# Performance work log

Hardware: AMD Instinct MI355X
Metric: run time of the kernel (lower is better)

## Reference

```python
import jax, jax.numpy as jnp
import numpy as np
from jax import lax

X_SIZE, Z_SIZE, H, GC, PD = 256, 64, 64, 16, 2
B, K, T = 256, 16, 50
LOG_SIG_MIN, LOG_SIG_MAX, LOG_P_MAX = -10.0, 10.0, 50.0
ZX = X_SIZE + Z_SIZE
LSTM_IN = ZX + PD


def setup_inputs() -> dict:
    key = jax.random.key(0)
    ks = jax.random.split(key, 24)
    s = lambda fan_in: 1.0 / np.sqrt(fan_in)
    u = lambda k, shape, sc: jax.random.uniform(k, shape, jnp.float32, -sc, sc)
    inp = {
        'x': jax.random.normal(ks[0], (B, X_SIZE), jnp.float32),
        'z_stacked': jax.random.normal(ks[1], (K, B, Z_SIZE), jnp.float32),
        'input_seqs': jax.random.normal(ks[2], (B, 8, 2, 2, 6), jnp.float32),
        'pred_seqs': jax.random.normal(ks[3], (B, T, 2, 2, 6), jnp.float32),
        # initial_h / initial_c linears: ZX -> H
        'Wh0': u(ks[4], (H, ZX), s(ZX)), 'bh0': u(ks[5], (H,), s(ZX)),
        'Wc0': u(ks[6], (H, ZX), s(ZX)), 'bc0': u(ks[7], (H,), s(ZX)),
        # LSTMCell: gates order i,f,g,o
        'Wih': u(ks[8], (4 * H, LSTM_IN), s(H)), 'Whh': u(ks[9], (4 * H, H), s(H)),
        'bih': u(ks[10], (4 * H,), s(H)), 'bhh': u(ks[11], (4 * H,), s(H)),
        # GMM parameter heads: H -> GC / GC*PD
        'Wpi': u(ks[12], (GC, H), s(H)), 'bpi': u(ks[13], (GC,), s(H)),
        'Wmu': u(ks[14], (GC * PD, H), s(H)), 'bmu': u(ks[15], (GC * PD,), s(H)),
        'Wls': u(ks[16], (GC * PD, H), s(H)), 'bls': u(ks[17], (GC * PD,), s(H)),
        'Wcorr': u(ks[18], (GC, H), s(H)), 'bcorr': u(ks[19], (GC,), s(H)),
        'n_z_samples': K,
    }
    return inp


def _gmm2d_log_prob(log_pis, mus, log_sigmas, corrs, value):
    # log_pis/corrs: [K,B,T,GC]; mus/log_sigmas: [K,B,T,GC*PD]; value: [B,T,PD]
    ls = jnp.clip(log_sigmas, LOG_SIG_MIN, LOG_SIG_MAX).reshape(K, B, T, GC, PD)
    mu = mus.reshape(K, B, T, GC, PD)
    dx = value[None, :, :, None, :] - mu                      # [K,B,T,GC,PD]
    zscore = dx * jnp.exp(-ls)                                # dx / sigma
    one_m_rho2 = 1.0 - corrs ** 2
    quad = (zscore[..., 0] ** 2 + zscore[..., 1] ** 2
            - 2.0 * corrs * zscore[..., 0] * zscore[..., 1])
    comp = (-jnp.log(2.0 * jnp.pi) - ls.sum(-1)
            - 0.5 * jnp.log(one_m_rho2) - 0.5 * quad / one_m_rho2)
    log_pi_n = jax.nn.log_softmax(log_pis, axis=-1)
    log_p_t = jax.nn.logsumexp(log_pi_n + comp, axis=-1)      # [K,B,T]
    return jnp.minimum(log_p_t, LOG_P_MAX)


def reference(x, z_stacked, input_seqs, pred_seqs,
              Wh0, bh0, Wc0, bc0, Wih, Whh, bih, bhh,
              Wpi, bpi, Wmu, bmu, Wls, bls, Wcorr, bcorr, n_z_samples):
    tgt_future = pred_seqs[:, :, 1, 1, 2:4]                   # [B,T,2]
    tgt_present = input_seqs[:, -1, 1, 1, 2:4]                # [B,2]
    z = z_stacked.reshape(-1, z_stacked.shape[-1])            # [K*B, z]
    zx = jnp.concatenate([z, jnp.tile(x, (n_z_samples, 1))], axis=1)  # [N, ZX]
    N = zx.shape[0]
    h0 = zx @ Wh0.T + bh0
    c0 = zx @ Wc0.T + bc0
    decode_inputs = jnp.concatenate([tgt_present[:, None, :], tgt_future[:, :T - 1, :]], axis=1)  # [B,T,2]
    inputs = jnp.concatenate([
        jnp.broadcast_to(zx[:, None, :], (N, T, ZX)),
        jnp.tile(decode_inputs, (n_z_samples, 1, 1))], axis=2)  # [N,T,ZX+2]

    def step(carry, xt):
        h, c = carry
        gates = xt @ Wih.T + bih + h @ Whh.T + bhh
        i, f, g, o = jnp.split(gates, 4, axis=-1)
        c = jax.nn.sigmoid(f) * c + jax.nn.sigmoid(i) * jnp.tanh(g)
        h = jax.nn.sigmoid(o) * jnp.tanh(c)
        return (h, c), h

    _, hs = lax.scan(step, (h0, c0), jnp.swapaxes(inputs, 0, 1))  # [T,N,H]
    hs = jnp.swapaxes(hs, 0, 1)                                   # [N,T,H]

    log_pis = (hs @ Wpi.T + bpi).reshape(K, B, T, GC)
    mus = (hs @ Wmu.T + bmu).reshape(K, B, T, GC * PD)
    log_sigmas = (hs @ Wls.T + bls).reshape(K, B, T, GC * PD)
    corrs = jnp.tanh(hs @ Wcorr.T + bcorr).reshape(K, B, T, GC)

    log_p_yt_xz = _gmm2d_log_prob(log_pis, mus, log_sigmas, corrs, tgt_future)
    return log_p_yt_xz.sum(axis=2)                                # [K,B]
```

## Files before the change

### kernel.cpp

```cpp
#include <hip/hip_runtime.h>


#define T_ 50

typedef __attribute__((ext_vector_type(8))) short short8;
typedef __attribute__((ext_vector_type(4))) float f32x4;

#define MFMA(a, b, c) __builtin_amdgcn_mfma_f32_16x16x32_bf16(a, b, c, 0, 0, 0)

#define HBYTES 26214400
#define WIH_B 0
#define WH0_B 20480
#define WC0_B 25600
#define WHH_B 30720
#define PRJ_B 34816

__device__ __forceinline__ float sigf(float x)  { return 1.0f / (1.0f + __expf(-x)); }
__device__ __forceinline__ float tanh_(float x) { return 1.0f - 2.0f / (__expf(2.0f * x) + 1.0f); }

__device__ __forceinline__ void splitf(float f, unsigned short& hi, unsigned short& lo) {
    unsigned b = __float_as_uint(f);
    hi = (unsigned short)(b >> 16);
    float fh = __uint_as_float(b & 0xffff0000u);
    lo = (unsigned short)(__float_as_uint(f - fh) >> 16);
}

__device__ __forceinline__ void pack8(const float* p, short8& hi, short8& lo) {
    #pragma unroll
    for (int e = 0; e < 8; ++e) {
        unsigned short h, l;
        splitf(p[e], h, l);
        hi[e] = (short)h; lo[e] = (short)l;
    }
}

__global__ void pack_kernel(const float* __restrict__ Wih, const float* __restrict__ Whh,
                            const float* __restrict__ Wh0, const float* __restrict__ Wc0,
                            const float* __restrict__ Wpi, const float* __restrict__ Wmu,
                            const float* __restrict__ Wls, const float* __restrict__ Wcorr,
                            short8* __restrict__ WF)
{
    int id = blockIdx.x * 256 + threadIdx.x;
    if (id >= 18176) return;
    const float* src;
    int dst0, dst1;
    if (id < 10240) {
        int ks = id >> 10, rem = id & 1023;
        int q = rem >> 8, rem2 = rem & 255;
        int w = rem2 >> 6, l = rem2 & 63;
        int g = l >> 4, c = l & 15;
        src = Wih + (q*64 + w*16 + c)*322 + ks*32 + g*8;
        dst0 = WIH_B + (((ks*4 + q)*2 + 0)*4 + w)*64 + l;
        dst1 = WIH_B + (((ks*4 + q)*2 + 1)*4 + w)*64 + l;
    } else if (id < 12800) {
        int t2 = id - 10240;
        int ks = t2 >> 8, rem = t2 & 255;
        int w = rem >> 6, l = rem & 63;
        int g = l >> 4, c = l & 15;
        src = Wh0 + (w*16 + c)*320 + ks*32 + g*8;
        dst0 = WH0_B + ((ks*2 + 0)*4 + w)*64 + l;
        dst1 = WH0_B + ((ks*2 + 1)*4 + w)*64 + l;
    } else if (id < 15360) {
        int t2 = id - 12800;
        int ks = t2 >> 8, rem = t2 & 255;
        int w = rem >> 6, l = rem & 63;
        int g = l >> 4, c = l & 15;
        src = Wc0 + (w*16 + c)*320 + ks*32 + g*8;
        dst0 = WC0_B + ((ks*2 + 0)*4 + w)*64 + l;
        dst1 = WC0_B + ((ks*2 + 1)*4 + w)*64 + l;
    } else if (id < 17408) {
        int t3 = id - 15360;
        int q = t3 >> 9, rem = t3 & 511;
        int ks = rem >> 8, rem2 = rem & 255;
        int w = rem2 >> 6, l = rem2 & 63;
        int g = l >> 4, c = l & 15;
        src = Whh + (q*64 + w*16 + c)*64 + ks*32 + g*8;
        dst0 = WHH_B + (((q*2 + ks)*2 + 0)*4 + w)*64 + l;
        dst1 = WHH_B + (((q*2 + ks)*2 + 1)*4 + w)*64 + l;
    } else {
        int t4 = id - 17408;
        int pt = t4 >> 7, rem = t4 & 127;
        int ks = rem >> 6, l = rem & 63;
        int g = l >> 4, c = l & 15;
        int r3 = pt*16 + c;
        const float* p;
        if      (r3 < 16) p = Wpi   + r3*64;
        else if (r3 < 48) p = Wmu   + (r3-16)*64;
        else if (r3 < 80) p = Wls   + (r3-48)*64;
        else              p = Wcorr + (r3-80)*64;
        src = p + ks*32 + g*8;
        dst0 = PRJ_B + ((pt*2 + ks)*2 + 0)*64 + l;
        dst1 = PRJ_B + ((pt*2 + ks)*2 + 1)*64 + l;
    }
    short8 hi, lo;
    pack8(src, hi, lo);
    WF[dst0] = hi;
    WF[dst1] = lo;
}

__launch_bounds__(256, 2)
__global__ void lstm_kernel(
    const float* __restrict__ x,        const float* __restrict__ z,
    const float* __restrict__ inp_seqs, const float* __restrict__ pred_seqs,
    const float* __restrict__ Wih,      const float* __restrict__ bh0,
    const float* __restrict__ bc0,      const float* __restrict__ bih,
    const float* __restrict__ bhh,
    unsigned short* __restrict__ Hout,  const short8* __restrict__ WF)
{
    __shared__ __align__(16) float smem[4560];
    float* ZXL = smem;
    unsigned short* HB = (unsigned short*)(smem + 2592);
    unsigned short* H0h = HB;
    unsigned short* H0l = HB + 576;
    unsigned short* H1h = HB + 1152;
    unsigned short* H1l = HB + 1728;
    float* FUT = smem + 3744;
    float* PRS = smem + 4544;

    const int j = threadIdx.x;
    const int w = j >> 6;
    const int l = j & 63;
    const int g = l >> 4;
    const int c = l & 15;
    const int U = w*16 + c;
    const int blk = blockIdx.x;

    for (int e = j; e < 8*320; e += 256) {
        int s = e / 320, k = e - s*320;
        int n = blk*8 + s, kk = n >> 8, b = n & 255;
        ZXL[s*324 + k] = (k < 64) ? z[(kk*256 + b)*64 + k] : x[b*256 + (k - 64)];
    }
    for (int e = j; e < T_*16; e += 256) {
        int t = e >> 4, s = (e >> 1) & 7;
        int b = (blk*8 + s) & 255;
        FUT[e] = pred_seqs[b*1200 + t*24 + 20 + (e & 1)];
    }
    if (j < 16) {
        int b = (blk*8 + (j >> 1)) & 255;
        PRS[j] = inp_seqs[b*192 + 188 + (j & 1)];
    }
    __syncthreads();

    const int R0 = U, R1 = 64+U, R2 = 128+U, R3 = 192+U;
    f32x4 gc[4], h0a, c0a;
    {
        float b0 = bih[R0]+bhh[R0], b1 = bih[R1]+bhh[R1];
        float b2 = bih[R2]+bhh[R2], b3 = bih[R3]+bhh[R3];
        gc[0] = (f32x4){b0,b0,b0,b0}; gc[1] = (f32x4){b1,b1,b1,b1};
        gc[2] = (f32x4){b2,b2,b2,b2}; gc[3] = (f32x4){b3,b3,b3,b3};
        float bh_ = bh0[U], bc_ = bc0[U];
        h0a = (f32x4){bh_,bh_,bh_,bh_};
        c0a = (f32x4){bc_,bc_,bc_,bc_};
    }
    for (int ks = 0; ks < 10; ++ks) {
        short8 ahi, alo;
        pack8(&ZXL[(c & 7)*324 + ks*32 + g*8], ahi, alo);
        #pragma unroll
        for (int q = 0; q < 4; ++q) {
            short8 Bh = WF[WIH_B + (((ks*4 + q)*2 + 0)*4 + w)*64 + l];
            short8 Bl = WF[WIH_B + (((ks*4 + q)*2 + 1)*4 + w)*64 + l];
            gc[q] = MFMA(ahi, Bh, gc[q]);
            gc[q] = MFMA(ahi, Bl, gc[q]);
            gc[q] = MFMA(alo, Bh, gc[q]);
        }
        {
            short8 Bh = WF[WH0_B + ((ks*2 + 0)*4 + w)*64 + l];
            short8 Bl = WF[WH0_B + ((ks*2 + 1)*4 + w)*64 + l];
            h0a = MFMA(ahi, Bh, h0a); h0a = MFMA(ahi, Bl, h0a); h0a = MFMA(alo, Bh, h0a);
        }
        {
            short8 Bh = WF[WC0_B + ((ks*2 + 0)*4 + w)*64 + l];
            short8 Bl = WF[WC0_B + ((ks*2 + 1)*4 + w)*64 + l];
            c0a = MFMA(ahi, Bh, c0a); c0a = MFMA(ahi, Bl, c0a); c0a = MFMA(alo, Bh, c0a);
        }
    }

    const bool lowg = (g < 2);
    const int s0 = 4*(g & 1) + (lowg ? 0 : 2);
    float cst0 = lowg ? c0a[0] : c0a[2];
    float cst1 = lowg ? c0a[1] : c0a[3];
    {
        float hv0 = lowg ? h0a[0] : h0a[2];
        float hv1 = lowg ? h0a[1] : h0a[3];
        unsigned short hh, ll;
        splitf(hv0, hh, ll); H0h[s0*72 + U] = hh; H0l[s0*72 + U] = ll;
        splitf(hv1, hh, ll); H0h[(s0+1)*72 + U] = hh; H0l[(s0+1)*72 + U] = ll;
    }

    float wd0[4], wd1[4];
    wd0[0] = Wih[R0*322+320]; wd1[0] = Wih[R0*322+321];
    wd0[1] = Wih[R1*322+320]; wd1[1] = Wih[R1*322+321];
    wd0[2] = Wih[R2*322+320]; wd1[2] = Wih[R2*322+321];
    wd0[3] = Wih[R3*322+320]; wd1[3] = Wih[R3*322+321];
    short8 WB[4][2][2];
    #pragma unroll
    for (int q = 0; q < 4; ++q)
        #pragma unroll
        for (int ks = 0; ks < 2; ++ks)
            #pragma unroll
            for (int p = 0; p < 2; ++p)
                WB[q][ks][p] = WF[WHH_B + (((q*2 + ks)*2 + p)*4 + w)*64 + l];

    __syncthreads();

    const int nbase = blk*8;
    for (int t = 0; t < T_; ++t) {
        const unsigned short* Hh = (t & 1) ? H1h : H0h;
        const unsigned short* Hl = (t & 1) ? H1l : H0l;
        unsigned short* Nh = (t & 1) ? H0h : H1h;
        unsigned short* Nl = (t & 1) ? H0l : H1l;

        short8 ah0 = *reinterpret_cast<const short8*>(Hh + (c & 7)*72 + g*8);
        short8 al0 = *reinterpret_cast<const short8*>(Hl + (c & 7)*72 + g*8);
        short8 ah1 = *reinterpret_cast<const short8*>(Hh + (c & 7)*72 + 32 + g*8);
        short8 al1 = *reinterpret_cast<const short8*>(Hl + (c & 7)*72 + 32 + g*8);

        const float* dptr = (t == 0) ? PRS : (FUT + (t-1)*16);
        float2 dvr[4];
        #pragma unroll
        for (int r = 0; r < 4; ++r)
            dvr[r] = *reinterpret_cast<const float2*>(dptr + ((4*g + r) & 7)*2);

        f32x4 aq[4];
        #pragma unroll
        for (int q = 0; q < 4; ++q) {
            #pragma unroll
            for (int r = 0; r < 4; ++r)
                aq[q][r] = gc[q][r] + dvr[r].x*wd0[q] + dvr[r].y*wd1[q];
            aq[q] = MFMA(ah0, WB[q][0][0], aq[q]);
            aq[q] = MFMA(ah0, WB[q][0][1], aq[q]);
            aq[q] = MFMA(al0, WB[q][0][0], aq[q]);
            aq[q] = MFMA(ah1, WB[q][1][0], aq[q]);
            aq[q] = MFMA(ah1, WB[q][1][1], aq[q]);
            aq[q] = MFMA(al1, WB[q][1][0], aq[q]);
        }

        float i0 = lowg ? aq[0][0] : aq[0][2], i1 = lowg ? aq[0][1] : aq[0][3];
        float f0 = lowg ? aq[1][0] : aq[1][2], f1 = lowg ? aq[1][1] : aq[1][3];
        float g0 = lowg ? aq[2][0] : aq[2][2], g1 = lowg ? aq[2][1] : aq[2][3];
        float o0 = lowg ? aq[3][0] : aq[3][2], o1 = lowg ? aq[3][1] : aq[3][3];
        float cc0 = sigf(f0)*cst0 + sigf(i0)*tanh_(g0); cst0 = cc0;
        float cc1 = sigf(f1)*cst1 + sigf(i1)*tanh_(g1); cst1 = cc1;
        float hv0 = sigf(o0)*tanh_(cc0);
        float hv1 = sigf(o1)*tanh_(cc1);

        unsigned short hh0, ll0, hh1, ll1;
        splitf(hv0, hh0, ll0);
        splitf(hv1, hh1, ll1);
        Hout[(size_t)(t*4096 + nbase + s0)*64 + U]     = hh0;
        Hout[(size_t)(t*4096 + nbase + s0 + 1)*64 + U] = hh1;
        Nh[s0*72 + U] = hh0;  Nl[s0*72 + U] = ll0;
        Nh[(s0+1)*72 + U] = hh1;  Nl[(s0+1)*72 + U] = ll1;
        __syncthreads();
    }
}

__launch_bounds__(256, 3)
__global__ void head_kernel(const float* __restrict__ pred_seqs,
                            const float* __restrict__ bpi, const float* __restrict__ bmu,
                            const float* __restrict__ bls, const float* __restrict__ bcorr,
                            const unsigned short* __restrict__ Hin,
                            const short8* __restrict__ WF,
                            float* __restrict__ out)
{
    __shared__ __align__(16) float PL[4][1600];
    const int j = threadIdx.x;
    const int w = j >> 6;
    const int l = j & 63;
    const int g = l >> 4;
    const int c = l & 15;
    const int blk = blockIdx.x;
    const int set = blk >> 2, chunk = blk & 3;
    const int t0 = (chunk*25) >> 1, t1 = ((chunk+1)*25) >> 1;

    float bias[6];
    #pragma unroll
    for (int pt = 0; pt < 6; ++pt) {
        int r3 = pt*16 + c;
        bias[pt] = (r3 < 16) ? bpi[r3] : (r3 < 48) ? bmu[r3-16]
                 : (r3 < 80) ? bls[r3-48] : bcorr[r3-80];
    }

    const int s = l >> 2, q4 = l & 3;
    const int n_s = set*16 + s, b_s = n_s & 255;
    float* PLw = &PL[w][0];
    float sum_local = 0.0f;

    for (int t = t0 + w; t < t1; t += 4) {
        const unsigned short* hp = Hin + (size_t)(t*4096 + set*16 + c)*64;
        short8 ah0 = *reinterpret_cast<const short8*>(hp + g*8);
        short8 ah1 = *reinterpret_cast<const short8*>(hp + 32 + g*8);
        #pragma unroll
        for (int pt = 0; pt < 6; ++pt) {
            short8 B00 = WF[PRJ_B + ((pt*2 + 0)*2 + 0)*64 + l];
            short8 B01 = WF[PRJ_B + ((pt*2 + 0)*2 + 1)*64 + l];
            short8 B10 = WF[PRJ_B + ((pt*2 + 1)*2 + 0)*64 + l];
            short8 B11 = WF[PRJ_B + ((pt*2 + 1)*2 + 1)*64 + l];
            f32x4 p = (f32x4){bias[pt], bias[pt], bias[pt], bias[pt]};
            p = MFMA(ah0, B00, p);
            p = MFMA(ah0, B01, p);
            p = MFMA(ah1, B10, p);
            p = MFMA(ah1, B11, p);
            #pragma unroll
            for (int r = 0; r < 4; ++r) PLw[(4*g + r)*100 + pt*16 + c] = p[r];
        }
        asm volatile("s_waitcnt lgkmcnt(0)" ::: "memory");
        __builtin_amdgcn_sched_barrier(0);

        float2 tv = *reinterpret_cast<const float2*>(pred_seqs + b_s*1200 + t*24 + 20);
        float a[4], m = -1e30f, Ppi = 0.0f;
        #pragma unroll
        for (int i = 0; i < 4; ++i) {
            int cq = q4*4 + i;
            float pi = PLw[s*100 + cq];
            float2 mu = *reinterpret_cast<const float2*>(PLw + s*100 + 16 + 2*cq);
            float2 ls = *reinterpret_cast<const float2*>(PLw + s*100 + 48 + 2*cq);
            float co = PLw[s*100 + 80 + cq];
            float l0 = fminf(fmaxf(ls.x, -10.0f), 10.0f);
            float l1 = fminf(fmaxf(ls.y, -10.0f), 10.0f);
            float z0 = (tv.x - mu.x) * __expf(-l0);
            float z1 = (tv.y - mu.y) * __expf(-l1);
            float ct = tanh_(co);
            float omr = 1.0f - ct*ct;
            float quad = z0*z0 + z1*z1 - 2.0f*ct*z0*z1;
            float comp = -1.8378770664093453f - (l0 + l1) - 0.5f*__logf(omr) - 0.5f*quad/omr;
            a[i] = pi + comp;
            m = fmaxf(m, a[i]);
            Ppi += __expf(pi);
        }
        m = fmaxf(m, __shfl_xor(m, 1));
        m = fmaxf(m, __shfl_xor(m, 2));
        float E = __expf(a[0]-m) + __expf(a[1]-m) + __expf(a[2]-m) + __expf(a[3]-m);
        E   += __shfl_xor(E, 1);   E   += __shfl_xor(E, 2);
        Ppi += __shfl_xor(Ppi, 1); Ppi += __shfl_xor(Ppi, 2);
        float logp = m + __logf(E) - __logf(Ppi);
        sum_local += fminf(logp, 50.0f);
    }
    if (q4 == 0) atomicAdd(out + n_s, sum_local);
}

extern "C" void kernel_launch(void* const* d_in, const int* in_sizes, int n_in,
                              void* d_out, int out_size, void* d_ws, size_t ws_size,
                              hipStream_t stream) {
    const float* x     = (const float*)d_in[0];
    const float* z     = (const float*)d_in[1];
    const float* iseq  = (const float*)d_in[2];
    const float* pseq  = (const float*)d_in[3];
    const float* Wh0   = (const float*)d_in[4];
    const float* bh0   = (const float*)d_in[5];
    const float* Wc0   = (const float*)d_in[6];
    const float* bc0   = (const float*)d_in[7];
    const float* Wih   = (const float*)d_in[8];
    const float* Whh   = (const float*)d_in[9];
    const float* bih   = (const float*)d_in[10];
    const float* bhh   = (const float*)d_in[11];
    const float* Wpi   = (const float*)d_in[12];
    const float* bpi   = (const float*)d_in[13];
    const float* Wmu   = (const float*)d_in[14];
    const float* bmu   = (const float*)d_in[15];
    const float* Wls   = (const float*)d_in[16];
    const float* bls   = (const float*)d_in[17];
    const float* Wcorr = (const float*)d_in[18];
    const float* bcorr = (const float*)d_in[19];
    float* out = (float*)d_out;

    unsigned short* Hbuf = (unsigned short*)d_ws;
    short8* WF = (short8*)((char*)d_ws + HBYTES);

    pack_kernel<<<71, 256, 0, stream>>>(Wih, Whh, Wh0, Wc0, Wpi, Wmu, Wls, Wcorr, WF);
    lstm_kernel<<<512, 256, 0, stream>>>(x, z, iseq, pseq, Wih, bh0, bc0, bih, bhh,
                                         Hbuf, (const short8*)WF);
    hipMemsetAsync(d_out, 0, 4096 * sizeof(float), stream);
    head_kernel<<<1024, 256, 0, stream>>>(pseq, bpi, bmu, bls, bcorr,
                                          (const unsigned short*)Hbuf,
                                          (const short8*)WF, out);
}
```

Measured before the change: 114.6 us.

## Split LSTM into prep GEMM kernel and per-wave recurrence without block barriers

Moves the input-projection and initial h/c GEMMs into a separate prep kernel that writes the gate constants, h0 and c0 to workspace, and packs only Whh and the head weights. The recurrence now gives each wave its own 4 sequences with all of Whh kept in registers, so the per-step __syncthreads is gone and only wave-local LDS sync remains. Each wave does 16 tiles of 6 MFMAs per step but uses only one row of each result, trading wasted MFMA work and heavy register pressure for no cross-wave synchronization. The recurrent grid halves to 256 blocks.

```diff
diff --git a/kernel.cpp b/kernel.cpp
--- a/kernel.cpp
+++ b/kernel.cpp
@@ -2,18 +2,16 @@
 
 
 #define T_ 50
-
 typedef __attribute__((ext_vector_type(8))) short short8;
 typedef __attribute__((ext_vector_type(4))) float f32x4;
-
-#define MFMA(a, b, c) __builtin_amdgcn_mfma_f32_16x16x32_bf16(a, b, c, 0, 0, 0)
-
-#define HBYTES 26214400
-#define WIH_B 0
-#define WH0_B 20480
-#define WC0_B 25600
-#define WHH_B 30720
-#define PRJ_B 34816
+#define MFMA(a,b,c) __builtin_amdgcn_mfma_f32_16x16x32_bf16(a,b,c,0,0,0)
+
+#define HOUT_B 0u
+#define GCT_B  26214400u
+#define H0_B   30408704u
+#define C0_B   31457280u
+#define WF_B   32505856u
+#define PRJ_SLOT 4096
 
 __device__ __forceinline__ float sigf(float x)  { return 1.0f / (1.0f + __expf(-x)); }
 __device__ __forceinline__ float tanh_(float x) { return 1.0f - 2.0f / (__expf(2.0f * x) + 1.0f); }
@@ -34,224 +32,209 @@
     }
 }
 
-__global__ void pack_kernel(const float* __restrict__ Wih, const float* __restrict__ Whh,
-                            const float* __restrict__ Wh0, const float* __restrict__ Wc0,
-                            const float* __restrict__ Wpi, const float* __restrict__ Wmu,
-                            const float* __restrict__ Wls, const float* __restrict__ Wcorr,
-                            short8* __restrict__ WF)
+union U8 { short8 s; unsigned u[4]; };
+
+__launch_bounds__(256, 1)
+__global__ void prep_kernel(
+    const float* __restrict__ x,   const float* __restrict__ z,
+    const float* __restrict__ Wh0, const float* __restrict__ bh0,
+    const float* __restrict__ Wc0, const float* __restrict__ bc0,
+    const float* __restrict__ Wih, const float* __restrict__ Whh,
+    const float* __restrict__ bih, const float* __restrict__ bhh,
+    const float* __restrict__ Wpi, const float* __restrict__ Wmu,
+    const float* __restrict__ Wls, const float* __restrict__ Wcorr,
+    float* __restrict__ gcT, unsigned* __restrict__ h0u32,
+    float* __restrict__ c0f, short8* __restrict__ WF)
 {
-    int id = blockIdx.x * 256 + threadIdx.x;
-    if (id >= 18176) return;
-    const float* src;
-    int dst0, dst1;
-    if (id < 10240) {
-        int ks = id >> 10, rem = id & 1023;
-        int q = rem >> 8, rem2 = rem & 255;
-        int w = rem2 >> 6, l = rem2 & 63;
-        int g = l >> 4, c = l & 15;
-        src = Wih + (q*64 + w*16 + c)*322 + ks*32 + g*8;
-        dst0 = WIH_B + (((ks*4 + q)*2 + 0)*4 + w)*64 + l;
-        dst1 = WIH_B + (((ks*4 + q)*2 + 1)*4 + w)*64 + l;
-    } else if (id < 12800) {
-        int t2 = id - 10240;
-        int ks = t2 >> 8, rem = t2 & 255;
-        int w = rem >> 6, l = rem & 63;
-        int g = l >> 4, c = l & 15;
-        src = Wh0 + (w*16 + c)*320 + ks*32 + g*8;
-        dst0 = WH0_B + ((ks*2 + 0)*4 + w)*64 + l;
-        dst1 = WH0_B + ((ks*2 + 1)*4 + w)*64 + l;
-    } else if (id < 15360) {
-        int t2 = id - 12800;
-        int ks = t2 >> 8, rem = t2 & 255;
-        int w = rem >> 6, l = rem & 63;
-        int g = l >> 4, c = l & 15;
-        src = Wc0 + (w*16 + c)*320 + ks*32 + g*8;
-        dst0 = WC0_B + ((ks*2 + 0)*4 + w)*64 + l;
-        dst1 = WC0_B + ((ks*2 + 1)*4 + w)*64 + l;
-    } else if (id < 17408) {
-        int t3 = id - 15360;
-        int q = t3 >> 9, rem = t3 & 511;
-        int ks = rem >> 8, rem2 = rem & 255;
-        int w = rem2 >> 6, l = rem2 & 63;
-        int g = l >> 4, c = l & 15;
-        src = Whh + (q*64 + w*16 + c)*64 + ks*32 + g*8;
-        dst0 = WHH_B + (((q*2 + ks)*2 + 0)*4 + w)*64 + l;
-        dst1 = WHH_B + (((q*2 + ks)*2 + 1)*4 + w)*64 + l;
-    } else {
-        int t4 = id - 17408;
-        int pt = t4 >> 7, rem = t4 & 127;
-        int ks = rem >> 6, l = rem & 63;
-        int g = l >> 4, c = l & 15;
-        int r3 = pt*16 + c;
-        const float* p;
-        if      (r3 < 16) p = Wpi   + r3*64;
-        else if (r3 < 48) p = Wmu   + (r3-16)*64;
-        else if (r3 < 80) p = Wls   + (r3-48)*64;
-        else              p = Wcorr + (r3-80)*64;
-        src = p + ks*32 + g*8;
-        dst0 = PRJ_B + ((pt*2 + ks)*2 + 0)*64 + l;
-        dst1 = PRJ_B + ((pt*2 + ks)*2 + 1)*64 + l;
-    }
-    short8 hi, lo;
-    pack8(src, hi, lo);
-    WF[dst0] = hi;
-    WF[dst1] = lo;
-}
-
-__launch_bounds__(256, 2)
+    const int j = threadIdx.x;
+    if (blockIdx.x >= 256) {
+        int tid = (blockIdx.x - 256)*256 + j;
+        if (tid < 2048) {
+            int lane = tid & 63, r = tid >> 6;
+            int ks = r & 1, tile = r >> 1;
+            int tau = tile >> 2, ublk = tile & 3;
+            int g = lane >> 4, c = lane & 15;
+            const float* src = Whh + (tau*64 + 16*ublk + c)*64 + ks*32 + g*8;
+            short8 hi, lo; pack8(src, hi, lo);
+            WF[(r*2 + 0)*64 + lane] = hi;
+            WF[(r*2 + 1)*64 + lane] = lo;
+        } else if (tid < 2816) {
+            int t2 = tid - 2048;
+            int lane = t2 & 63, r = t2 >> 6;
+            int ks = r & 1, pt = r >> 1;
+            int g = lane >> 4, c = lane & 15;
+            int r3 = pt*16 + c;
+            const float* p;
+            if      (r3 < 16) p = Wpi   + r3*64;
+            else if (r3 < 48) p = Wmu   + (r3-16)*64;
+            else if (r3 < 80) p = Wls   + (r3-48)*64;
+            else              p = Wcorr + (r3-80)*64;
+            short8 hi, lo; pack8(p + ks*32 + g*8, hi, lo);
+            WF[PRJ_SLOT + (r*2 + 0)*64 + lane] = hi;
+            WF[PRJ_SLOT + (r*2 + 1)*64 + lane] = lo;
+        }
+        return;
+    }
+
+    __shared__ __align__(16) float ZXL[16*324];
+    const int blk = blockIdx.x;
+    for (int e = j; e < 16*320; e += 256) {
+        int s = e / 320, k = e - s*320;
+        int n = blk*16 + s, b = n & 255;
+        ZXL[s*324 + k] = (k < 64) ? z[n*64 + k] : x[b*256 + (k - 64)];
+    }
+    __syncthreads();
+
+    const int w = j >> 6, l = j & 63, g = l >> 4, c = l & 15;
+    f32x4 acc[6];
+    const float* src[6];
+    #pragma unroll
+    for (int i = 0; i < 6; ++i) {
+        int T = w*6 + i;
+        float bias;
+        if (T < 16)      { int ga = T*16 + c;      bias = bih[ga] + bhh[ga]; src[i] = Wih + ga*322; }
+        else if (T < 20) { int u  = (T-16)*16 + c; bias = bh0[u];            src[i] = Wh0 + u*320; }
+        else             { int u  = (T-20)*16 + c; bias = bc0[u];            src[i] = Wc0 + u*320; }
+        acc[i] = (f32x4){bias, bias, bias, bias};
+    }
+    for (int ks = 0; ks < 10; ++ks) {
+        short8 ah, al;
+        pack8(&ZXL[c*324 + ks*32 + g*8], ah, al);
+        #pragma unroll
+        for (int i = 0; i < 6; ++i) {
+            short8 bh, bl;
+            pack8(src[i] + ks*32 + g*8, bh, bl);
+            acc[i] = MFMA(ah, bh, acc[i]);
+            acc[i] = MFMA(ah, bl, acc[i]);
+            acc[i] = MFMA(al, bh, acc[i]);
+        }
+    }
+    #pragma unroll
+    for (int i = 0; i < 6; ++i) {
+        int T = w*6 + i;
+        if (T < 16) {
+            *reinterpret_cast<f32x4*>(gcT + (T*16 + c)*4096 + blk*16 + 4*g) = acc[i];
+        } else if (T < 20) {
+            int u = (T-16)*16 + c;
+            #pragma unroll
+            for (int r = 0; r < 4; ++r) {
+                unsigned short hh, ll; splitf(acc[i][r], hh, ll);
+                h0u32[(blk*16 + 4*g + r)*64 + u] = ((unsigned)hh << 16) | ll;
+            }
+        } else {
+            int u = (T-20)*16 + c;
+            #pragma unroll
+            for (int r = 0; r < 4; ++r)
+                c0f[(blk*16 + 4*g + r)*64 + u] = acc[i][r];
+        }
+    }
+}
+
+__launch_bounds__(256, 1)
 __global__ void lstm_kernel(
-    const float* __restrict__ x,        const float* __restrict__ z,
     const float* __restrict__ inp_seqs, const float* __restrict__ pred_seqs,
-    const float* __restrict__ Wih,      const float* __restrict__ bh0,
-    const float* __restrict__ bc0,      const float* __restrict__ bih,
-    const float* __restrict__ bhh,
-    unsigned short* __restrict__ Hout,  const short8* __restrict__ WF)
+    const float* __restrict__ Wih,
+    const float* __restrict__ gcT, const unsigned* __restrict__ h0u32,
+    const float* __restrict__ c0f, unsigned short* __restrict__ Hout,
+    const short8* __restrict__ WF)
 {
-    __shared__ __align__(16) float smem[4560];
-    float* ZXL = smem;
-    unsigned short* HB = (unsigned short*)(smem + 2592);
-    unsigned short* H0h = HB;
-    unsigned short* H0l = HB + 576;
-    unsigned short* H1h = HB + 1152;
-    unsigned short* H1l = HB + 1728;
-    float* FUT = smem + 3744;
-    float* PRS = smem + 4544;
-
+    __shared__ unsigned HLs[4][16*65];
+    __shared__ float    DQs[4][51*8];
     const int j = threadIdx.x;
-    const int w = j >> 6;
-    const int l = j & 63;
-    const int g = l >> 4;
-    const int c = l & 15;
-    const int U = w*16 + c;
-    const int blk = blockIdx.x;
-
-    for (int e = j; e < 8*320; e += 256) {
-        int s = e / 320, k = e - s*320;
-        int n = blk*8 + s, kk = n >> 8, b = n & 255;
-        ZXL[s*324 + k] = (k < 64) ? z[(kk*256 + b)*64 + k] : x[b*256 + (k - 64)];
-    }
-    for (int e = j; e < T_*16; e += 256) {
-        int t = e >> 4, s = (e >> 1) & 7;
-        int b = (blk*8 + s) & 255;
-        FUT[e] = pred_seqs[b*1200 + t*24 + 20 + (e & 1)];
-    }
-    if (j < 16) {
-        int b = (blk*8 + (j >> 1)) & 255;
-        PRS[j] = inp_seqs[b*192 + 188 + (j & 1)];
-    }
-    __syncthreads();
-
-    const int R0 = U, R1 = 64+U, R2 = 128+U, R3 = 192+U;
-    f32x4 gc[4], h0a, c0a;
-    {
-        float b0 = bih[R0]+bhh[R0], b1 = bih[R1]+bhh[R1];
-        float b2 = bih[R2]+bhh[R2], b3 = bih[R3]+bhh[R3];
-        gc[0] = (f32x4){b0,b0,b0,b0}; gc[1] = (f32x4){b1,b1,b1,b1};
-        gc[2] = (f32x4){b2,b2,b2,b2}; gc[3] = (f32x4){b3,b3,b3,b3};
-        float bh_ = bh0[U], bc_ = bc0[U];
-        h0a = (f32x4){bh_,bh_,bh_,bh_};
-        c0a = (f32x4){bc_,bc_,bc_,bc_};
-    }
-    for (int ks = 0; ks < 10; ++ks) {
-        short8 ahi, alo;
-        pack8(&ZXL[(c & 7)*324 + ks*32 + g*8], ahi, alo);
+    const int wv = j >> 6, l = j & 63, g = l >> 4, c = l & 15;
+    unsigned* HL = HLs[wv];
+    float* DQ = DQs[wv];
+    const int nb = blockIdx.x*16 + wv*4;
+
+    for (int e = l; e < 16*65; e += 64) HL[e] = 0u;
+    for (int e = l; e < 51*8; e += 64) {
+        int t = e >> 3, rem = e & 7, s = rem >> 1, comp = rem & 1;
+        int b = (nb + s) & 255;
+        DQ[e] = (t == 0) ? inp_seqs[b*192 + 188 + comp]
+                         : pred_seqs[b*1200 + (t-1)*24 + 20 + comp];
+    }
+
+    short8 WB[4][4][2][2];
+    #pragma unroll
+    for (int tau = 0; tau < 4; ++tau)
+        #pragma unroll
+        for (int ub = 0; ub < 4; ++ub)
+            #pragma unroll
+            for (int ks = 0; ks < 2; ++ks)
+                #pragma unroll
+                for (int p = 0; p < 2; ++p)
+                    WB[tau][ub][ks][p] = WF[(((tau*4 + ub)*2 + ks)*2 + p)*64 + l];
+
+    float gcs[16];
+    #pragma unroll
+    for (int T = 0; T < 16; ++T) gcs[T] = gcT[(T*16 + c)*4096 + nb + g];
+
+    float wd0[4][4], wd1[4][4];
+    #pragma unroll
+    for (int tau = 0; tau < 4; ++tau)
+        #pragma unroll
+        for (int ub = 0; ub < 4; ++ub) {
+            int ga = tau*64 + 16*ub + c;
+            wd0[tau][ub] = Wih[ga*322 + 320];
+            wd1[tau][ub] = Wih[ga*322 + 321];
+        }
+
+    float cst[4];
+    #pragma unroll
+    for (int ub = 0; ub < 4; ++ub) {
+        cst[ub] = c0f[(nb + g)*64 + 16*ub + c];
+        HL[(4*g)*65 + 16*ub + c] = h0u32[(nb + g)*64 + 16*ub + c];
+    }
+    asm volatile("s_waitcnt lgkmcnt(0)" ::: "memory");
+
+    const f32x4 zero4 = (f32x4){0.0f, 0.0f, 0.0f, 0.0f};
+
+    for (int t = 0; t < T_; ++t) {
+        unsigned hv[16];
+        #pragma unroll
+        for (int e = 0; e < 8; ++e) hv[e]     = HL[c*65 + 8*g + e];
+        #pragma unroll
+        for (int e = 0; e < 8; ++e) hv[8 + e] = HL[c*65 + 32 + 8*g + e];
+        U8 A0h, A0l, A1h, A1l;
         #pragma unroll
         for (int q = 0; q < 4; ++q) {
-            short8 Bh = WF[WIH_B + (((ks*4 + q)*2 + 0)*4 + w)*64 + l];
-            short8 Bl = WF[WIH_B + (((ks*4 + q)*2 + 1)*4 + w)*64 + l];
-            gc[q] = MFMA(ahi, Bh, gc[q]);
-            gc[q] = MFMA(ahi, Bl, gc[q]);
-            gc[q] = MFMA(alo, Bh, gc[q]);
-        }
-        {
-            short8 Bh = WF[WH0_B + ((ks*2 + 0)*4 + w)*64 + l];
-            short8 Bl = WF[WH0_B + ((ks*2 + 1)*4 + w)*64 + l];
-            h0a = MFMA(ahi, Bh, h0a); h0a = MFMA(ahi, Bl, h0a); h0a = MFMA(alo, Bh, h0a);
-        }
-        {
-            short8 Bh = WF[WC0_B + ((ks*2 + 0)*4 + w)*64 + l];
-            short8 Bl = WF[WC0_B + ((ks*2 + 1)*4 + w)*64 + l];
-            c0a = MFMA(ahi, Bh, c0a); c0a = MFMA(ahi, Bl, c0a); c0a = MFMA(alo, Bh, c0a);
-        }
-    }
-
-    const bool lowg = (g < 2);
-    const int s0 = 4*(g & 1) + (lowg ? 0 : 2);
-    float cst0 = lowg ? c0a[0] : c0a[2];
-    float cst1 = lowg ? c0a[1] : c0a[3];
-    {
-        float hv0 = lowg ? h0a[0] : h0a[2];
-        float hv1 = lowg ? h0a[1] : h0a[3];
-        unsigned short hh, ll;
-        splitf(hv0, hh, ll); H0h[s0*72 + U] = hh; H0l[s0*72 + U] = ll;
-        splitf(hv1, hh, ll); H0h[(s0+1)*72 + U] = hh; H0l[(s0+1)*72 + U] = ll;
-    }
-
-    float wd0[4], wd1[4];
-    wd0[0] = Wih[R0*322+320]; wd1[0] = Wih[R0*322+321];
-    wd0[1] = Wih[R1*322+320]; wd1[1] = Wih[R1*322+321];
-    wd0[2] = Wih[R2*322+320]; wd1[2] = Wih[R2*322+321];
-    wd0[3] = Wih[R3*322+320]; wd1[3] = Wih[R3*322+321];
-    short8 WB[4][2][2];
-    #pragma unroll
-    for (int q = 0; q < 4; ++q)
-        #pragma unroll
-        for (int ks = 0; ks < 2; ++ks)
-            #pragma unroll
-            for (int p = 0; p < 2; ++p)
-                WB[q][ks][p] = WF[WHH_B + (((q*2 + ks)*2 + p)*4 + w)*64 + l];
-
-    __syncthreads();
-
-    const int nbase = blk*8;
-    for (int t = 0; t < T_; ++t) {
-        const unsigned short* Hh = (t & 1) ? H1h : H0h;
-        const unsigned short* Hl = (t & 1) ? H1l : H0l;
-        unsigned short* Nh = (t & 1) ? H0h : H1h;
-        unsigned short* Nl = (t & 1) ? H0l : H1l;
-
-        short8 ah0 = *reinterpret_cast<const short8*>(Hh + (c & 7)*72 + g*8);
-        short8 al0 = *reinterpret_cast<const short8*>(Hl + (c & 7)*72 + g*8);
-        short8 ah1 = *reinterpret_cast<const short8*>(Hh + (c & 7)*72 + 32 + g*8);
-        short8 al1 = *reinterpret_cast<const short8*>(Hl + (c & 7)*72 + 32 + g*8);
-
-        const float* dptr = (t == 0) ? PRS : (FUT + (t-1)*16);
-        float2 dvr[4];
-        #pragma unroll
-        for (int r = 0; r < 4; ++r)
-            dvr[r] = *reinterpret_cast<const float2*>(dptr + ((4*g + r) & 7)*2);
-
-        f32x4 aq[4];
-        #pragma unroll
-        for (int q = 0; q < 4; ++q) {
-            #pragma unroll
-            for (int r = 0; r < 4; ++r)
-                aq[q][r] = gc[q][r] + dvr[r].x*wd0[q] + dvr[r].y*wd1[q];
-            aq[q] = MFMA(ah0, WB[q][0][0], aq[q]);
-            aq[q] = MFMA(ah0, WB[q][0][1], aq[q]);
-            aq[q] = MFMA(al0, WB[q][0][0], aq[q]);
-            aq[q] = MFMA(ah1, WB[q][1][0], aq[q]);
-            aq[q] = MFMA(ah1, WB[q][1][1], aq[q]);
-            aq[q] = MFMA(al1, WB[q][1][0], aq[q]);
-        }
-
-        float i0 = lowg ? aq[0][0] : aq[0][2], i1 = lowg ? aq[0][1] : aq[0][3];
-        float f0 = lowg ? aq[1][0] : aq[1][2], f1 = lowg ? aq[1][1] : aq[1][3];
-        float g0 = lowg ? aq[2][0] : aq[2][2], g1 = lowg ? aq[2][1] : aq[2][3];
-        float o0 = lowg ? aq[3][0] : aq[3][2], o1 = lowg ? aq[3][1] : aq[3][3];
-        float cc0 = sigf(f0)*cst0 + sigf(i0)*tanh_(g0); cst0 = cc0;
-        float cc1 = sigf(f1)*cst1 + sigf(i1)*tanh_(g1); cst1 = cc1;
-        float hv0 = sigf(o0)*tanh_(cc0);
-        float hv1 = sigf(o1)*tanh_(cc1);
-
-        unsigned short hh0, ll0, hh1, ll1;
-        splitf(hv0, hh0, ll0);
-        splitf(hv1, hh1, ll1);
-        Hout[(size_t)(t*4096 + nbase + s0)*64 + U]     = hh0;
-        Hout[(size_t)(t*4096 + nbase + s0 + 1)*64 + U] = hh1;
-        Nh[s0*72 + U] = hh0;  Nl[s0*72 + U] = ll0;
-        Nh[(s0+1)*72 + U] = hh1;  Nl[(s0+1)*72 + U] = ll1;
-        __syncthreads();
+            A0h.u[q] = (hv[2*q] >> 16)      | (hv[2*q+1] & 0xffff0000u);
+            A0l.u[q] = (hv[2*q] & 0xffffu)  | (hv[2*q+1] << 16);
+            A1h.u[q] = (hv[8+2*q] >> 16)     | (hv[8+2*q+1] & 0xffff0000u);
+            A1l.u[q] = (hv[8+2*q] & 0xffffu) | (hv[8+2*q+1] << 16);
+        }
+
+        float2 dv = *reinterpret_cast<const float2*>(&DQ[t*8 + g*2]);
+
+        float gv[4][4];
+        #pragma unroll
+        for (int tau = 0; tau < 4; ++tau) {
+            #pragma unroll
+            for (int ub = 0; ub < 4; ++ub) {
+                f32x4 a = MFMA(A0h.s, WB[tau][ub][0][0], zero4);
+                a = MFMA(A0l.s, WB[tau][ub][0][0], a);
+                a = MFMA(A0h.s, WB[tau][ub][0][1], a);
+                a = MFMA(A1h.s, WB[tau][ub][1][0], a);
+                a = MFMA(A1l.s, WB[tau][ub][1][0], a);
+                a = MFMA(A1h.s, WB[tau][ub][1][1], a);
+                gv[tau][ub] = a[0] + gcs[tau*4 + ub];
+            }
+        }
+
+        #pragma unroll
+        for (int ub = 0; ub < 4; ++ub) {
+            float iv = gv[0][ub] + dv.x*wd0[0][ub] + dv.y*wd1[0][ub];
+            float fv = gv[1][ub] + dv.x*wd0[1][ub] + dv.y*wd1[1][ub];
+            float gg = gv[2][ub] + dv.x*wd0[2][ub] + dv.y*wd1[2][ub];
+            float ov = gv[3][ub] + dv.x*wd0[3][ub] + dv.y*wd1[3][ub];
+            float cc = sigf(fv)*cst[ub] + sigf(iv)*tanh_(gg);
+            cst[ub] = cc;
+            float hn = sigf(ov)*tanh_(cc);
+            unsigned short hh, ll; splitf(hn, hh, ll);
+            HL[(4*g)*65 + 16*ub + c] = ((unsigned)hh << 16) | ll;
+            Hout[(size_t)(t*4096 + nb + g)*64 + 16*ub + c] = hh;
+        }
+        asm volatile("s_waitcnt lgkmcnt(0)" ::: "memory");
     }
 }
 
@@ -292,10 +275,10 @@
         short8 ah1 = *reinterpret_cast<const short8*>(hp + 32 + g*8);
         #pragma unroll
         for (int pt = 0; pt < 6; ++pt) {
-            short8 B00 = WF[PRJ_B + ((pt*2 + 0)*2 + 0)*64 + l];
-            short8 B01 = WF[PRJ_B + ((pt*2 + 0)*2 + 1)*64 + l];
-            short8 B10 = WF[PRJ_B + ((pt*2 + 1)*2 + 0)*64 + l];
-            short8 B11 = WF[PRJ_B + ((pt*2 + 1)*2 + 1)*64 + l];
+            short8 B00 = WF[PRJ_SLOT + ((pt*2 + 0)*2 + 0)*64 + l];
+            short8 B01 = WF[PRJ_SLOT + ((pt*2 + 0)*2 + 1)*64 + l];
+            short8 B10 = WF[PRJ_SLOT + ((pt*2 + 1)*2 + 0)*64 + l];
+            short8 B11 = WF[PRJ_SLOT + ((pt*2 + 1)*2 + 1)*64 + l];
             f32x4 p = (f32x4){bias[pt], bias[pt], bias[pt], bias[pt]};
             p = MFMA(ah0, B00, p);
             p = MFMA(ah0, B01, p);
@@ -364,14 +347,20 @@
     const float* bcorr = (const float*)d_in[19];
     float* out = (float*)d_out;
 
-    unsigned short* Hbuf = (unsigned short*)d_ws;
-    short8* WF = (short8*)((char*)d_ws + HBYTES);
-
-    pack_kernel<<<71, 256, 0, stream>>>(Wih, Whh, Wh0, Wc0, Wpi, Wmu, Wls, Wcorr, WF);
-    lstm_kernel<<<512, 256, 0, stream>>>(x, z, iseq, pseq, Wih, bh0, bc0, bih, bhh,
-                                         Hbuf, (const short8*)WF);
+    char* ws = (char*)d_ws;
+    unsigned short* Hout = (unsigned short*)(ws + HOUT_B);
+    float*    gcT   = (float*)(ws + GCT_B);
+    unsigned* h0u32 = (unsigned*)(ws + H0_B);
+    float*    c0f   = (float*)(ws + C0_B);
+    short8*   WF    = (short8*)(ws + WF_B);
+
+    prep_kernel<<<267, 256, 0, stream>>>(x, z, Wh0, bh0, Wc0, bc0, Wih, Whh,
+                                         bih, bhh, Wpi, Wmu, Wls, Wcorr,
+                                         gcT, h0u32, c0f, WF);
     hipMemsetAsync(d_out, 0, 4096 * sizeof(float), stream);
+    lstm_kernel<<<256, 256, 0, stream>>>(iseq, pseq, Wih, gcT, h0u32, c0f,
+                                         Hout, (const short8*)WF);
     head_kernel<<<1024, 256, 0, stream>>>(pseq, bpi, bmu, bls, bcorr,
-                                          (const unsigned short*)Hbuf,
+                                          (const unsigned short*)Hout,
                                           (const short8*)WF, out);
 }
```

Result: slower. 159.1 us (+38.9%).
